# Optimization experiments

Measured on AMD Instinct MI355X. Metric: run time of the kernel, lower is better.

The kernel has to match this reference:

```python
import jax, jax.numpy as jnp
import numpy as np

N = 64      # num_neighbors + 1
H = 512     # hidden_size
T = 1024    # history length


def setup_inputs() -> dict:
    key = jax.random.key(0)
    ks = jax.random.split(key, 10)
    s = 1.0 / np.sqrt(H)  # PyTorch LSTM/Linear init scale
    return {
        "in_recent_values": jax.random.normal(ks[0], (N,), dtype=jnp.float32),
        "in_reputation_history": jax.random.normal(ks[1], (N, T), dtype=jnp.float32),
        # per-module LSTM params (input_size=1), gate order i,f,g,o
        "W_ih": jax.random.uniform(ks[2], (N, 4 * H), jnp.float32, -s, s),      # [N,4H] (input_size=1 squeezed)
        "W_hh": jax.random.uniform(ks[3], (N, 4 * H, H), jnp.float32, -s, s),   # [N,4H,H]
        "b_ih": jax.random.uniform(ks[4], (N, 4 * H), jnp.float32, -s, s),
        "b_hh": jax.random.uniform(ks[5], (N, 4 * H), jnp.float32, -s, s),
        # per-module output Linear(H+1 -> 1)
        "lin_W": jax.random.uniform(ks[6], (N, H + 1), jnp.float32, -s, s),
        "lin_b": jax.random.uniform(ks[7], (N,), jnp.float32, -s, s),
        # final Linear(N -> 1)
        "final_W": jax.random.uniform(ks[8], (N,), jnp.float32, -1.0 / np.sqrt(N), 1.0 / np.sqrt(N)),
        "final_b": jax.random.uniform(ks[9], (1,), jnp.float32, -1.0 / np.sqrt(N), 1.0 / np.sqrt(N)),
    }


def _batched_lstm_last_h(history, W_ih, W_hh, b_ih, b_hh):
    # history: [N,T]. Precompute input contribution for all steps: [T,N,4H]
    x_proj = history[:, :, None] * W_ih[:, None, :] + (b_ih + b_hh)[:, None, :]
    x_proj = jnp.swapaxes(x_proj, 0, 1)  # [T,N,4H]

    def step(carry, x_t):
        h, c = carry  # [N,H] each
        gates = x_t + jnp.einsum("nh,ngh->ng", h, W_hh)  # [N,4H]
        i, f, g, o = jnp.split(gates, 4, axis=-1)
        i = jax.nn.sigmoid(i)
        f = jax.nn.sigmoid(f)
        g = jnp.tanh(g)
        o = jax.nn.sigmoid(o)
        c = f * c + i * g
        h = o * jnp.tanh(c)
        return (h, c), None

    h0 = jnp.zeros((N, H), dtype=history.dtype)
    (h_last, _), _ = jax.lax.scan(step, (h0, h0), x_proj)
    return h_last  # [N,H]


def reference(in_recent_values, in_reputation_history, W_ih, W_hh, b_ih, b_hh,
              lin_W, lin_b, final_W, final_b):
    h_last = _batched_lstm_last_h(in_reputation_history, W_ih, W_hh, b_ih, b_hh)
    # per-module linear on [h_last, current_reading] -> scalar each
    feat = jnp.concatenate([h_last, in_recent_values[:, None]], axis=1)  # [N,H+1]
    per_mod = jnp.sum(feat * lin_W, axis=1) + lin_b                      # [N]
    out = per_mod @ final_W + final_b                                    # [1]
    return out
```

## Files before the change

### kernel.cpp

```cpp
#include <hip/hip_runtime.h>
#include <hip/hip_fp16.h>
#include <cstddef>

#define NMOD 64
#define HID 512
#define TSTEPS 1024
#define G4 2048

#define WOFF_PERMOD 0
#define WOFF_HX     16384
#define WOFF_W16    524288
#define W16_BYTES   ((size_t)NMOD * G4 * HID * 2)
#define WS_NEED     (WOFF_W16 + W16_BYTES)

typedef _Float16 half8_t __attribute__((ext_vector_type(8)));
typedef float    f32x4_t __attribute__((ext_vector_type(4)));

__device__ __forceinline__ float fsig(float x)  { return 1.0f / (1.0f + __expf(-x)); }
__device__ __forceinline__ float ftanh_(float x){ return 1.0f - 2.0f / (__expf(2.0f * x) + 1.0f); }

__device__ __forceinline__ half8_t h8(uint4 u) { return __builtin_bit_cast(half8_t, u); }

#define MFMA_F16(a, b, c) __builtin_amdgcn_mfma_f32_16x16x32_f16((a), (b), (c), 0, 0, 0)

__global__ __launch_bounds__(256) void conv_frag_kernel(const float* __restrict__ src,
                                                        unsigned* __restrict__ dst) {
    const unsigned t_lin = blockIdx.x * 256 + threadIdx.x;
    const unsigned chunk = t_lin >> 6, u = t_lin & 63;
    const unsigned l = ((u & 3) << 4) | (u >> 2);
    const unsigned t = (chunk << 6) | l;

    const int ll = t & 63;
    const int j  = (t >> 6) & 15;
    const int mt = (t >> 10) & 3;
    const int w  = (t >> 12) & 7;
    const int b  = (t >> 15) & 3;
    const int m  = (int)(t >> 17);
    const int kc = (4 * b + j) & 15;
    const int g  = ll >> 4, r16 = ll & 15;
    const int lr = w * 64 + mt * 16 + r16;
    const int gr = (lr >> 7) * 512 + b * 128 + (lr & 127);

    const float* sp = src + ((size_t)m * G4 + gr) * HID + kc * 32 + g * 8;
    const float4 a = *reinterpret_cast<const float4*>(sp);
    const float4 c = *reinterpret_cast<const float4*>(sp + 4);
    __half2 h0 = __floats2half2_rn(a.x, a.y);
    __half2 h1 = __floats2half2_rn(a.z, a.w);
    __half2 h2 = __floats2half2_rn(c.x, c.y);
    __half2 h3 = __floats2half2_rn(c.z, c.w);
    uint4 o;
    o.x = *reinterpret_cast<unsigned*>(&h0);
    o.y = *reinterpret_cast<unsigned*>(&h1);
    o.z = *reinterpret_cast<unsigned*>(&h2);
    o.w = *reinterpret_cast<unsigned*>(&h3);
    *reinterpret_cast<uint4*>(dst + (size_t)t * 4) = o;
}

__global__
__attribute__((amdgpu_flat_work_group_size(512, 512), amdgpu_waves_per_eu(2, 2)))
void lstm_mfma_kernel(
    const float* __restrict__ recent,
    const float* __restrict__ history,
    const float* __restrict__ W_ih,
    const float* __restrict__ b_ih,
    const float* __restrict__ b_hh,
    const float* __restrict__ lin_W,
    const float* __restrict__ lin_b,
    const unsigned* __restrict__ wf,
    unsigned long long* hx,
    float* __restrict__ per_mod)
{
    const int bid = blockIdx.x;
    const int m = (bid & 7) * 8 + (bid >> 5);
    const int b = (bid >> 3) & 3;
    const int tid = threadIdx.x;
    const int w   = tid >> 6;
    const int l   = tid & 63;
    const int g   = l >> 4;
    const int c16 = l & 15;

    __shared__ uint4 w_lds[8][4][4][64];
    __shared__ unsigned h_pk[256];
    __shared__ float gates_sh[512];
    __shared__ float hist_sh[TSTEPS];
    __shared__ float red_sh[8];

    for (int i = tid; i < TSTEPS; i += 512)
        hist_sh[i] = history[(size_t)m * TSTEPS + i];

    const uint4* fb = (const uint4*)wf + (size_t)((m * 4 + b) * 8 + w) * 4096;
    uint4 wr[4][12];
    #pragma unroll
    for (int mt = 0; mt < 4; ++mt)
        #pragma unroll
        for (int j = 0; j < 12; ++j)
            wr[mt][j] = fb[(mt * 16 + j) * 64 + l];
    #pragma unroll
    for (int mt = 0; mt < 4; ++mt)
        #pragma unroll
        for (int j2 = 0; j2 < 4; ++j2)
            w_lds[w][mt][j2][l] = fb[(mt * 16 + 12 + j2) * 64 + l];

    float wib4[4], bias4[4];
    if (c16 < 4) {
        #pragma unroll
        for (int e = 0; e < 4; ++e) {
            const int lr = w * 64 + c16 * 16 + g * 4 + e;
            const int gr = (lr >> 7) * 512 + b * 128 + (lr & 127);
            wib4[e]  = W_ih[(size_t)m * G4 + gr];
            bias4[e] = b_ih[(size_t)m * G4 + gr] + b_hh[(size_t)m * G4 + gr];
        }
    }

    const bool is_writer = (tid < 128);
    const bool is_reader = (tid >= 128 && tid < 320);
    const int  rr   = tid - 128;
    const int  widx = (((b + 1 + (rr >> 6)) & 3) << 6) + (rr & 63);

    float c0 = 0.0f;
    if (tid < 256) h_pk[tid] = 0u;
    __syncthreads();

    if (c16 < 4) {
        const float x0 = hist_sh[0];
        float4 o;
        o.x = x0 * wib4[0] + bias4[0];
        o.y = x0 * wib4[1] + bias4[1];
        o.z = x0 * wib4[2] + bias4[2];
        o.w = x0 * wib4[3] + bias4[3];
        *reinterpret_cast<float4*>(&gates_sh[w * 64 + c16 * 16 + g * 4]) = o;
    }

    for (int t = 0; t < TSTEPS - 1; ++t) {
        __syncthreads();
        const unsigned seq = (unsigned)(t + 1);
        const size_t pbase = (size_t)(seq & 1) * (NMOD * 256) + (size_t)m * 256;

        unsigned long long pv = 0;
        if (is_writer) {
            const float gi = fsig(gates_sh[tid]);
            const float gf = fsig(gates_sh[128 + tid]);
            const float gg = ftanh_(gates_sh[256 + tid]);
            const float go = fsig(gates_sh[384 + tid]);
            c0 = gf * c0 + gi * gg;
            const float hv = go * ftanh_(c0);
            const float ho = __shfl_xor(hv, 1, 64);
            if ((tid & 1) == 0) {
                __half2 hh = __floats2half2_rn(hv, ho);
                const unsigned pay = *reinterpret_cast<unsigned*>(&hh);
                const int word = tid >> 1;
                __hip_atomic_store(&hx[pbase + b * 64 + word],
                                   ((unsigned long long)seq << 32) | pay,
                                   __ATOMIC_RELAXED, __HIP_MEMORY_SCOPE_AGENT);
                h_pk[b * 64 + word] = pay;
            }
        } else if (is_reader) {
            pv = __hip_atomic_load(&hx[pbase + widx],
                                   __ATOMIC_RELAXED, __HIP_MEMORY_SCOPE_AGENT);
        }
        __syncthreads();

        f32x4_t acc0 = {0.f, 0.f, 0.f, 0.f};
        f32x4_t acc1 = {0.f, 0.f, 0.f, 0.f};
        f32x4_t acc2 = {0.f, 0.f, 0.f, 0.f};
        f32x4_t acc3 = {0.f, 0.f, 0.f, 0.f};

        #pragma unroll
        for (int j = 0; j < 4; ++j) {
            const int kc = 4 * b + j;
            const half8_t hv8 = h8(*(const uint4*)&h_pk[kc * 16 + g * 4]);
            acc0 = MFMA_F16(h8(wr[0][j]), hv8, acc0);
            acc1 = MFMA_F16(h8(wr[1][j]), hv8, acc1);
            acc2 = MFMA_F16(h8(wr[2][j]), hv8, acc2);
            acc3 = MFMA_F16(h8(wr[3][j]), hv8, acc3);
        }

        if (is_reader) {
            while ((unsigned)(pv >> 32) != seq)
                pv = __hip_atomic_load(&hx[pbase + widx],
                                       __ATOMIC_RELAXED, __HIP_MEMORY_SCOPE_AGENT);
            h_pk[widx] = (unsigned)pv;
        }
        __syncthreads();

        #pragma unroll
        for (int j = 4; j < 12; ++j) {
            const int kc = (4 * b + j) & 15;
            const half8_t hv8 = h8(*(const uint4*)&h_pk[kc * 16 + g * 4]);
            acc0 = MFMA_F16(h8(wr[0][j]), hv8, acc0);
            acc1 = MFMA_F16(h8(wr[1][j]), hv8, acc1);
            acc2 = MFMA_F16(h8(wr[2][j]), hv8, acc2);
            acc3 = MFMA_F16(h8(wr[3][j]), hv8, acc3);
        }
        #pragma unroll
        for (int j2 = 0; j2 < 4; ++j2) {
            const int kc = (4 * b + 12 + j2) & 15;
            const half8_t hv8 = h8(*(const uint4*)&h_pk[kc * 16 + g * 4]);
            acc0 = MFMA_F16(h8(w_lds[w][0][j2][l]), hv8, acc0);
            acc1 = MFMA_F16(h8(w_lds[w][1][j2][l]), hv8, acc1);
            acc2 = MFMA_F16(h8(w_lds[w][2][j2][l]), hv8, acc2);
            acc3 = MFMA_F16(h8(w_lds[w][3][j2][l]), hv8, acc3);
        }

        if (c16 < 4) {
            const f32x4_t a = (c16 == 0) ? acc0 : (c16 == 1) ? acc1
                             : (c16 == 2) ? acc2 : acc3;
            const float x1 = hist_sh[t + 1];
            float4 o;
            o.x = a[0] + x1 * wib4[0] + bias4[0];
            o.y = a[1] + x1 * wib4[1] + bias4[1];
            o.z = a[2] + x1 * wib4[2] + bias4[2];
            o.w = a[3] + x1 * wib4[3] + bias4[3];
            *reinterpret_cast<float4*>(&gates_sh[w * 64 + c16 * 16 + g * 4]) = o;
        }
    }

    __syncthreads();
    {
        const unsigned seq = (unsigned)TSTEPS;
        const size_t pbase = (size_t)(seq & 1) * (NMOD * 256) + (size_t)m * 256;
        if (is_writer) {
            const float gi = fsig(gates_sh[tid]);
            const float gf = fsig(gates_sh[128 + tid]);
            const float gg = ftanh_(gates_sh[256 + tid]);
            const float go = fsig(gates_sh[384 + tid]);
            c0 = gf * c0 + gi * gg;
            const float hv = go * ftanh_(c0);
            const float ho = __shfl_xor(hv, 1, 64);
            if ((tid & 1) == 0) {
                __half2 hh = __floats2half2_rn(hv, ho);
                const unsigned pay = *reinterpret_cast<unsigned*>(&hh);
                const int word = tid >> 1;
                __hip_atomic_store(&hx[pbase + b * 64 + word],
                                   ((unsigned long long)seq << 32) | pay,
                                   __ATOMIC_RELAXED, __HIP_MEMORY_SCOPE_AGENT);
                h_pk[b * 64 + word] = pay;
            }
        }
        if (b == 0) {
            if (is_reader) {
                unsigned long long pv;
                do {
                    pv = __hip_atomic_load(&hx[pbase + widx],
                                           __ATOMIC_RELAXED, __HIP_MEMORY_SCOPE_AGENT);
                } while ((unsigned)(pv >> 32) != seq);
                h_pk[widx] = (unsigned)pv;
            }
            __syncthreads();
            float v = 0.0f;
            if (tid < 256) {
                const __half2 u = *reinterpret_cast<const __half2*>(&h_pk[tid]);
                const float* lwp = lin_W + (size_t)m * (HID + 1);
                v = __half2float(u.x) * lwp[2 * tid] + __half2float(u.y) * lwp[2 * tid + 1];
            }
            #pragma unroll
            for (int s2 = 32; s2; s2 >>= 1) v += __shfl_xor(v, s2, 64);
            if ((tid & 63) == 0) red_sh[tid >> 6] = v;
            __syncthreads();
            if (tid == 0) {
                float s = 0.0f;
                #pragma unroll
                for (int wv2 = 0; wv2 < 8; ++wv2) s += red_sh[wv2];
                s += recent[m] * lin_W[(size_t)m * (HID + 1) + HID] + lin_b[m];
                per_mod[m] = s;
            }
        }
    }
}

__global__ __launch_bounds__(1024) void lstm_module_kernel(
    const float* __restrict__ recent,
    const float* __restrict__ history,
    const float* __restrict__ W_ih,
    const float* __restrict__ W_hh,
    const float* __restrict__ b_ih,
    const float* __restrict__ b_hh,
    const float* __restrict__ lin_W,
    const float* __restrict__ lin_b,
    float* __restrict__ per_mod)
{
    const int n = blockIdx.x;
    const int tid = threadIdx.x;

    __shared__ float h_sh[HID];
    __shared__ float gates_sh[G4];
    __shared__ float wib_sh[G4];
    __shared__ float bias_sh[G4];
    __shared__ float hist_sh[TSTEPS];

    for (int i = tid; i < G4; i += 1024) {
        wib_sh[i]  = W_ih[(size_t)n * G4 + i];
        bias_sh[i] = b_ih[(size_t)n * G4 + i] + b_hh[(size_t)n * G4 + i];
    }
    for (int i = tid; i < TSTEPS; i += 1024) hist_sh[i] = history[(size_t)n * TSTEPS + i];
    if (tid < HID) h_sh[tid] = 0.0f;
    float c_reg = 0.0f;
    __syncthreads();

    const int sub = tid & 15;
    const int rid = tid >> 4;
    const float* Wbase = W_hh + (size_t)n * G4 * HID;

    for (int t = 0; t < TSTEPS; ++t) {
        const float x = hist_sh[t];
        float hreg[32];
        #pragma unroll
        for (int j = 0; j < 8; ++j) {
            const float4 hv = *reinterpret_cast<const float4*>(&h_sh[sub * 4 + j * 64]);
            hreg[4 * j + 0] = hv.x; hreg[4 * j + 1] = hv.y;
            hreg[4 * j + 2] = hv.z; hreg[4 * j + 3] = hv.w;
        }
        for (int p = 0; p < 32; ++p) {
            const int r = p * 64 + rid;
            const float* wr = Wbase + (size_t)r * HID + sub * 4;
            float acc = 0.0f;
            #pragma unroll
            for (int j = 0; j < 8; ++j) {
                const float4 wv = *reinterpret_cast<const float4*>(wr + j * 64);
                acc += wv.x * hreg[4*j+0] + wv.y * hreg[4*j+1]
                     + wv.z * hreg[4*j+2] + wv.w * hreg[4*j+3];
            }
            acc += __shfl_xor(acc, 1, 64);
            acc += __shfl_xor(acc, 2, 64);
            acc += __shfl_xor(acc, 4, 64);
            acc += __shfl_xor(acc, 8, 64);
            if (sub == 0) gates_sh[r] = acc + x * wib_sh[r] + bias_sh[r];
        }
        __syncthreads();
        if (tid < HID) {
            const float ig = fsig(gates_sh[tid]);
            const float fg = fsig(gates_sh[HID + tid]);
            const float gg = ftanh_(gates_sh[2 * HID + tid]);
            const float og = fsig(gates_sh[3 * HID + tid]);
            c_reg = fg * c_reg + ig * gg;
            h_sh[tid] = og * ftanh_(c_reg);
        }
        __syncthreads();
    }

    if (tid < HID) {
        float v = h_sh[tid] * lin_W[(size_t)n * (HID + 1) + tid];
        #pragma unroll
        for (int m2 = 32; m2; m2 >>= 1) v += __shfl_xor(v, m2, 64);
        if ((tid & 63) == 0) gates_sh[tid >> 6] = v;
    }
    __syncthreads();
    if (tid == 0) {
        float s = 0.0f;
        #pragma unroll
        for (int w = 0; w < HID / 64; ++w) s += gates_sh[w];
        s += recent[n] * lin_W[(size_t)n * (HID + 1) + HID] + lin_b[n];
        per_mod[n] = s;
    }
}

__global__ void finish_kernel(const float* __restrict__ per_mod,
                              const float* __restrict__ final_W,
                              const float* __restrict__ final_b,
                              float* __restrict__ out)
{
    const int l = threadIdx.x;
    float v = per_mod[l] * final_W[l];
    #pragma unroll
    for (int m = 32; m; m >>= 1) v += __shfl_xor(v, m, 64);
    if (l == 0) out[0] = v + final_b[0];
}

extern "C" void kernel_launch(void* const* d_in, const int* in_sizes, int n_in,
                              void* d_out, int out_size, void* d_ws, size_t ws_size,
                              hipStream_t stream) {
    const float* recent  = (const float*)d_in[0];
    const float* history = (const float*)d_in[1];
    const float* W_ih    = (const float*)d_in[2];
    const float* W_hh    = (const float*)d_in[3];
    const float* b_ih    = (const float*)d_in[4];
    const float* b_hh    = (const float*)d_in[5];
    const float* lin_W   = (const float*)d_in[6];
    const float* lin_b   = (const float*)d_in[7];
    const float* final_W = (const float*)d_in[8];
    const float* final_b = (const float*)d_in[9];
    float* out = (float*)d_out;
    float* per_mod = (float*)d_ws;

    if (ws_size >= WS_NEED) {
        unsigned* wfrag = (unsigned*)((char*)d_ws + WOFF_W16);
        unsigned long long* hx = (unsigned long long*)((char*)d_ws + WOFF_HX);

        hipMemsetAsync(d_ws, 0, WOFF_W16, stream);

        conv_frag_kernel<<<32768, 256, 0, stream>>>(W_hh, wfrag);

        lstm_mfma_kernel<<<NMOD * 4, 512, 0, stream>>>(
            recent, history, W_ih, b_ih, b_hh, lin_W, lin_b,
            wfrag, hx, per_mod);
    } else {
        lstm_module_kernel<<<NMOD, 1024, 0, stream>>>(
            recent, history, W_ih, W_hh, b_ih, b_hh, lin_W, lin_b, per_mod);
    }
    finish_kernel<<<1, 64, 0, stream>>>(per_mod, final_W, final_b, out);
}
```

Measured before the change: 2.509 ms.

## Replace block barriers with per-wave h staging and spin-waits in LSTM step

Each wave now polls the global exchange buffer itself for all 256 h words and writes them into a private LDS staging slice. This removes two __syncthreads per timestep, and each wave starts its local-slice MFMAs once its own block's words arrive. s_setprio raises priority around the MFMA sections. The cost is 8x redundant atomic loads of the exchange buffer and more global polling traffic. The local slice is also read back from global memory instead of being written directly to LDS.

```diff
diff --git a/kernel.cpp b/kernel.cpp
--- a/kernel.cpp
+++ b/kernel.cpp
@@ -22,6 +22,7 @@
 __device__ __forceinline__ half8_t h8(uint4 u) { return __builtin_bit_cast(half8_t, u); }
 
 #define MFMA_F16(a, b, c) __builtin_amdgcn_mfma_f32_16x16x32_f16((a), (b), (c), 0, 0, 0)
+#define ALOAD(p) __hip_atomic_load((p), __ATOMIC_RELAXED, __HIP_MEMORY_SCOPE_AGENT)
 
 __global__ __launch_bounds__(256) void conv_frag_kernel(const float* __restrict__ src,
                                                         unsigned* __restrict__ dst) {
@@ -80,7 +81,7 @@
     const int c16 = l & 15;
 
     __shared__ uint4 w_lds[8][4][4][64];
-    __shared__ unsigned h_pk[256];
+    __shared__ unsigned h_stage[8][256];
     __shared__ float gates_sh[512];
     __shared__ float hist_sh[TSTEPS];
     __shared__ float red_sh[8];
@@ -112,13 +113,12 @@
         }
     }
 
-    const bool is_writer = (tid < 128);
-    const bool is_reader = (tid >= 128 && tid < 320);
-    const int  rr   = tid - 128;
-    const int  widx = (((b + 1 + (rr >> 6)) & 3) << 6) + (rr & 63);
+    const int wloc = (b << 6) + l;
+    const int wr0  = (((b + 1) & 3) << 6) + l;
+    const int wr1  = (((b + 2) & 3) << 6) + l;
+    const int wr2  = (((b + 3) & 3) << 6) + l;
 
     float c0 = 0.0f;
-    if (tid < 256) h_pk[tid] = 0u;
     __syncthreads();
 
     if (c16 < 4) {
@@ -136,8 +136,7 @@
         const unsigned seq = (unsigned)(t + 1);
         const size_t pbase = (size_t)(seq & 1) * (NMOD * 256) + (size_t)m * 256;
 
-        unsigned long long pv = 0;
-        if (is_writer) {
+        if (tid < 128) {
             const float gi = fsig(gates_sh[tid]);
             const float gf = fsig(gates_sh[128 + tid]);
             const float gg = ftanh_(gates_sh[256 + tid]);
@@ -148,45 +147,50 @@
             if ((tid & 1) == 0) {
                 __half2 hh = __floats2half2_rn(hv, ho);
                 const unsigned pay = *reinterpret_cast<unsigned*>(&hh);
-                const int word = tid >> 1;
-                __hip_atomic_store(&hx[pbase + b * 64 + word],
+                __hip_atomic_store(&hx[pbase + b * 64 + (tid >> 1)],
                                    ((unsigned long long)seq << 32) | pay,
                                    __ATOMIC_RELAXED, __HIP_MEMORY_SCOPE_AGENT);
-                h_pk[b * 64 + word] = pay;
-            }
-        } else if (is_reader) {
-            pv = __hip_atomic_load(&hx[pbase + widx],
-                                   __ATOMIC_RELAXED, __HIP_MEMORY_SCOPE_AGENT);
-        }
-        __syncthreads();
+            }
+        }
+
+        unsigned long long a0 = ALOAD(&hx[pbase + wloc]);
+        unsigned long long r0 = ALOAD(&hx[pbase + wr0]);
+        unsigned long long r1 = ALOAD(&hx[pbase + wr1]);
+        unsigned long long r2 = ALOAD(&hx[pbase + wr2]);
+        while ((unsigned)(a0 >> 32) != seq) a0 = ALOAD(&hx[pbase + wloc]);
+        h_stage[w][wloc] = (unsigned)a0;
 
         f32x4_t acc0 = {0.f, 0.f, 0.f, 0.f};
         f32x4_t acc1 = {0.f, 0.f, 0.f, 0.f};
         f32x4_t acc2 = {0.f, 0.f, 0.f, 0.f};
         f32x4_t acc3 = {0.f, 0.f, 0.f, 0.f};
-
+        __builtin_amdgcn_s_setprio(1);
         #pragma unroll
         for (int j = 0; j < 4; ++j) {
             const int kc = 4 * b + j;
-            const half8_t hv8 = h8(*(const uint4*)&h_pk[kc * 16 + g * 4]);
+            const half8_t hv8 = h8(*(const uint4*)&h_stage[w][kc * 16 + g * 4]);
             acc0 = MFMA_F16(h8(wr[0][j]), hv8, acc0);
             acc1 = MFMA_F16(h8(wr[1][j]), hv8, acc1);
             acc2 = MFMA_F16(h8(wr[2][j]), hv8, acc2);
             acc3 = MFMA_F16(h8(wr[3][j]), hv8, acc3);
         }
-
-        if (is_reader) {
-            while ((unsigned)(pv >> 32) != seq)
-                pv = __hip_atomic_load(&hx[pbase + widx],
-                                       __ATOMIC_RELAXED, __HIP_MEMORY_SCOPE_AGENT);
-            h_pk[widx] = (unsigned)pv;
-        }
-        __syncthreads();
-
+        __builtin_amdgcn_s_setprio(0);
+
+        while ((unsigned)(r0 >> 32) != seq || (unsigned)(r1 >> 32) != seq ||
+               (unsigned)(r2 >> 32) != seq) {
+            if ((unsigned)(r0 >> 32) != seq) r0 = ALOAD(&hx[pbase + wr0]);
+            if ((unsigned)(r1 >> 32) != seq) r1 = ALOAD(&hx[pbase + wr1]);
+            if ((unsigned)(r2 >> 32) != seq) r2 = ALOAD(&hx[pbase + wr2]);
+        }
+        h_stage[w][wr0] = (unsigned)r0;
+        h_stage[w][wr1] = (unsigned)r1;
+        h_stage[w][wr2] = (unsigned)r2;
+
+        __builtin_amdgcn_s_setprio(1);
         #pragma unroll
         for (int j = 4; j < 12; ++j) {
             const int kc = (4 * b + j) & 15;
-            const half8_t hv8 = h8(*(const uint4*)&h_pk[kc * 16 + g * 4]);
+            const half8_t hv8 = h8(*(const uint4*)&h_stage[w][kc * 16 + g * 4]);
             acc0 = MFMA_F16(h8(wr[0][j]), hv8, acc0);
             acc1 = MFMA_F16(h8(wr[1][j]), hv8, acc1);
             acc2 = MFMA_F16(h8(wr[2][j]), hv8, acc2);
@@ -195,12 +199,13 @@
         #pragma unroll
         for (int j2 = 0; j2 < 4; ++j2) {
             const int kc = (4 * b + 12 + j2) & 15;
-            const half8_t hv8 = h8(*(const uint4*)&h_pk[kc * 16 + g * 4]);
+            const half8_t hv8 = h8(*(const uint4*)&h_stage[w][kc * 16 + g * 4]);
             acc0 = MFMA_F16(h8(w_lds[w][0][j2][l]), hv8, acc0);
             acc1 = MFMA_F16(h8(w_lds[w][1][j2][l]), hv8, acc1);
             acc2 = MFMA_F16(h8(w_lds[w][2][j2][l]), hv8, acc2);
             acc3 = MFMA_F16(h8(w_lds[w][3][j2][l]), hv8, acc3);
         }
+        __builtin_amdgcn_s_setprio(0);
 
         if (c16 < 4) {
             const f32x4_t a = (c16 == 0) ? acc0 : (c16 == 1) ? acc1
@@ -219,7 +224,7 @@
     {
         const unsigned seq = (unsigned)TSTEPS;
         const size_t pbase = (size_t)(seq & 1) * (NMOD * 256) + (size_t)m * 256;
-        if (is_writer) {
+        if (tid < 128) {
             const float gi = fsig(gates_sh[tid]);
             const float gf = fsig(gates_sh[128 + tid]);
             const float gg = ftanh_(gates_sh[256 + tid]);
@@ -230,26 +235,23 @@
             if ((tid & 1) == 0) {
                 __half2 hh = __floats2half2_rn(hv, ho);
                 const unsigned pay = *reinterpret_cast<unsigned*>(&hh);
-                const int word = tid >> 1;
-                __hip_atomic_store(&hx[pbase + b * 64 + word],
+                __hip_atomic_store(&hx[pbase + b * 64 + (tid >> 1)],
                                    ((unsigned long long)seq << 32) | pay,
                                    __ATOMIC_RELAXED, __HIP_MEMORY_SCOPE_AGENT);
-                h_pk[b * 64 + word] = pay;
             }
         }
         if (b == 0) {
-            if (is_reader) {
+            if (tid < 256) {
                 unsigned long long pv;
                 do {
-                    pv = __hip_atomic_load(&hx[pbase + widx],
-                                           __ATOMIC_RELAXED, __HIP_MEMORY_SCOPE_AGENT);
+                    pv = ALOAD(&hx[pbase + tid]);
                 } while ((unsigned)(pv >> 32) != seq);
-                h_pk[widx] = (unsigned)pv;
+                h_stage[0][tid] = (unsigned)pv;
             }
             __syncthreads();
             float v = 0.0f;
             if (tid < 256) {
-                const __half2 u = *reinterpret_cast<const __half2*>(&h_pk[tid]);
+                const __half2 u = *reinterpret_cast<const __half2*>(&h_stage[0][tid]);
                 const float* lwp = lin_W + (size_t)m * (HID + 1);
                 v = __half2float(u.x) * lwp[2 * tid] + __half2float(u.y) * lwp[2 * tid + 1];
             }
@@ -312,11 +314,11 @@
         }
         for (int p = 0; p < 32; ++p) {
             const int r = p * 64 + rid;
-            const float* wr = Wbase + (size_t)r * HID + sub * 4;
+            const float* wrp = Wbase + (size_t)r * HID + sub * 4;
             float acc = 0.0f;
             #pragma unroll
             for (int j = 0; j < 8; ++j) {
-                const float4 wv = *reinterpret_cast<const float4*>(wr + j * 64);
+                const float4 wv = *reinterpret_cast<const float4*>(wrp + j * 64);
                 acc += wv.x * hreg[4*j+0] + wv.y * hreg[4*j+1]
                      + wv.z * hreg[4*j+2] + wv.w * hreg[4*j+3];
             }
```

Result: slower. 3.790 ms (+51.1%).
